# Kernel tuning notes

Hardware: AMD Instinct MI355X
Metric: run time of the kernel (lower is better)

Reference implementation:

```python
import jax, jax.numpy as jnp
import numpy as np

N = 30000      # nodes of type 'A'
IN = 128       # in_channels = hidden*2
H = 64         # hidden_channels
OUT = 64
M = 4          # number of metapaths (seq len for attention)
E = 480000     # edges per relation
NH = 8         # num_heads
HD = OUT // NH # head dim = 8
FF = 2048      # transformer dim_feedforward (torch default)
L = 2          # transformer layers
EPS = 1e-5


def setup_inputs() -> dict:
    key = jax.random.key(0)
    ks = iter(jax.random.split(key, 64))
    nk = lambda: next(ks)
    rn = lambda shape, s=0.05: (jax.random.normal(nk(), shape, jnp.float32) * s)
    x = jax.random.normal(nk(), (N, IN), jnp.float32)
    edge_index = jax.random.randint(nk(), (M, 2, E), 0, N, dtype=jnp.int32)
    counts = jnp.array([3.0, 1.0, 2.0, 2.0], jnp.float32)
    mp_weights = counts / counts.sum()
    inp = dict(x=x, edge_index=edge_index, mp_weights=mp_weights,
               W0=rn((M, H, IN)), b0=rn((M, H)), Wl=rn((M, H, IN)), bl=rn((M, H)),
               W1=rn((M, H, IN)), b1=rn((M, H)), Wo=rn((M, OUT, H)), bo=rn((M, OUT)),
               tinw=rn((L, 3 * OUT, OUT)), tinb=rn((L, 3 * OUT)),
               tow=rn((L, OUT, OUT)), tob=rn((L, OUT)),
               ln1g=jnp.ones((L, OUT)), ln1b=jnp.zeros((L, OUT)),
               ff1w=rn((L, FF, OUT)), ff1b=rn((L, FF)),
               ff2w=rn((L, OUT, FF)), ff2b=rn((L, OUT)),
               ln2g=jnp.ones((L, OUT)), ln2b=jnp.zeros((L, OUT)),
               r1w=rn((OUT, OUT)), r1b=rn((OUT,)), r2w=rn((1, OUT)), r2b=rn((1,)))
    return inp


def _layer_norm(v, g, b):
    mu = v.mean(-1, keepdims=True)
    var = ((v - mu) ** 2).mean(-1, keepdims=True)
    return (v - mu) / jnp.sqrt(var + EPS) * g + b


def reference(x, edge_index, mp_weights, W0, b0, Wl, bl, W1, b1, Wo, bo,
              tinw, tinb, tow, tob, ln1g, ln1b, ff1w, ff1b, ff2w, ff2b,
              ln2g, ln2b, r1w, r1b, r2w, r2b):
    n = x.shape[0]
    # ---- per-metapath GNN: gather + scatter-add + 3 fused linears ----
    embs = []
    for m in range(M):
        src, dst = edge_index[m, 0], edge_index[m, 1]
        # flow='target_to_source', aggr='add': agg[i] = sum_{e: src[e]==i} h[dst[e]]
        agg = jnp.zeros_like(x).at[src].add(x[dst])
        # w_l(agg) + w_0(h) + w_1(x), with h == x (forward passes x=h=h_dict[dst])
        h = jax.nn.relu(agg @ Wl[m].T + bl[m] + x @ (W0[m] + W1[m]).T + (b0[m] + b1[m]))
        embs.append(h @ Wo[m].T + bo[m])  # out_proj on updated start-type feats
    e = jnp.stack(embs, axis=1) * mp_weights[None, :, None]  # (N, M, OUT)

    # ---- 2-layer post-norm TransformerEncoder (batch_first, eval/no dropout) ----
    for l in range(L):
        qkv = e @ tinw[l].T + tinb[l]                       # (N, M, 3*OUT)
        q, k, v = jnp.split(qkv, 3, axis=-1)
        split = lambda t: t.reshape(n, M, NH, HD).transpose(0, 2, 1, 3)  # (N,NH,M,HD)
        q, k, v = split(q), split(k), split(v)
        attn = jax.nn.softmax(jnp.einsum('nhqd,nhkd->nhqk', q, k) / np.float32(np.sqrt(HD)), axis=-1)
        o = jnp.einsum('nhqk,nhkd->nhqd', attn, v).transpose(0, 2, 1, 3).reshape(n, M, OUT)
        o = o @ tow[l].T + tob[l]
        e = _layer_norm(e + o, ln1g[l], ln1b[l])
        f = jax.nn.relu(e @ ff1w[l].T + ff1b[l]) @ ff2w[l].T + ff2b[l]
        e = _layer_norm(e + f, ln2g[l], ln2b[l])

    pooled = e.mean(axis=1)                                  # (N, OUT)
    out = jax.nn.relu(pooled @ r1w.T + r1b) @ r2w.T + r2b    # (N, 1)
    return out[:, 0]
```

## Files before the change

### kernel.cpp

```cpp
#include <hip/hip_runtime.h>
#include <hip/hip_bf16.h>
#include <math.h>

#define N_NODES 30000
#define M_P     4
#define E_EDGES 480000
#define N_TOK   (N_NODES * 4)
#define N_ROWS  (M_P * N_NODES)
#define SLOTS   62
#define LN_EPS  1e-5f

typedef short bf16x8 __attribute__((ext_vector_type(8)));
typedef float f32x4  __attribute__((ext_vector_type(4)));
#define MFMA_B16(a, b, c) __builtin_amdgcn_mfma_f32_16x16x32_bf16(a, b, c, 0, 0, 0)

__device__ inline unsigned short f2bf(float f) {
    union { float f; unsigned u; } v; v.f = f;
    unsigned r = v.u + 0x7fffu + ((v.u >> 16) & 1u);
    return (unsigned short)(r >> 16);
}
__device__ inline unsigned pack2bf(float a, float b) {
    union { __hip_bfloat162 h; unsigned u; } cv;
    cv.h = __float22bfloat162_rn(make_float2(a, b));
    return cv.u;
}
__device__ inline float bf2f(short s) {
    union { unsigned u; float f; } v; v.u = ((unsigned)(unsigned short)s) << 16;
    return v.f;
}

__global__ __launch_bounds__(256, 2) void k_lin_yz(
    const float* __restrict__ x,
    const float* __restrict__ W0, const float* __restrict__ b0,
    const float* __restrict__ Wl, const float* __restrict__ bl,
    const float* __restrict__ W1, const float* __restrict__ b1,
    float* __restrict__ y, float* __restrict__ z)
{
    __shared__ float xT[128][68];
    __shared__ float wT[128][68];
    const int t     = threadIdx.x;
    const int m     = blockIdx.y >> 1;
    const int which = blockIdx.y & 1;
    const int node0 = blockIdx.x * 64;

    #pragma unroll
    for (int i = 0; i < 8; ++i) {
        const int node = (t & 31) + 32 * (i & 1);
        const int kq   = (t >> 5) + 8 * (i >> 1);
        float4 v = make_float4(0.f, 0.f, 0.f, 0.f);
        const int n = node0 + node;
        if (n < N_NODES) v = *(const float4*)(x + n * 128 + kq * 4);
        xT[kq * 4 + 0][node] = v.x; xT[kq * 4 + 1][node] = v.y;
        xT[kq * 4 + 2][node] = v.z; xT[kq * 4 + 3][node] = v.w;
    }
    #pragma unroll
    for (int i = 0; i < 8; ++i) {
        const int h  = (t & 31) + 32 * (i & 1);
        const int kq = (t >> 5) + 8 * (i >> 1);
        float4 v;
        if (which) {
            v = *(const float4*)(W0 + (m * 64 + h) * 128 + kq * 4);
            const float4 v2 = *(const float4*)(W1 + (m * 64 + h) * 128 + kq * 4);
            v.x += v2.x; v.y += v2.y; v.z += v2.z; v.w += v2.w;
        } else {
            v = *(const float4*)(Wl + (m * 64 + h) * 128 + kq * 4);
        }
        wT[kq * 4 + 0][h] = v.x; wT[kq * 4 + 1][h] = v.y;
        wT[kq * 4 + 2][h] = v.z; wT[kq * 4 + 3][h] = v.w;
    }
    __syncthreads();

    const int tx = t & 15, ty = t >> 4;
    const int hb = tx * 4, nb = ty * 4;
    float acc[4][4] = {};
    #pragma unroll 8
    for (int k = 0; k < 128; ++k) {
        const float4 a = *(const float4*)&xT[k][nb];
        const float4 b = *(const float4*)&wT[k][hb];
        acc[0][0] += a.x * b.x; acc[0][1] += a.x * b.y; acc[0][2] += a.x * b.z; acc[0][3] += a.x * b.w;
        acc[1][0] += a.y * b.x; acc[1][1] += a.y * b.y; acc[1][2] += a.y * b.z; acc[1][3] += a.y * b.w;
        acc[2][0] += a.z * b.x; acc[2][1] += a.z * b.y; acc[2][2] += a.z * b.z; acc[2][3] += a.z * b.w;
        acc[3][0] += a.w * b.x; acc[3][1] += a.w * b.y; acc[3][2] += a.w * b.z; acc[3][3] += a.w * b.w;
    }
    float bias[4] = {0.f, 0.f, 0.f, 0.f};
    if (which) {
        #pragma unroll
        for (int j = 0; j < 4; ++j)
            bias[j] = b0[m * 64 + hb + j] + b1[m * 64 + hb + j] + bl[m * 64 + hb + j];
    }
    float* outp = which ? z : y;
    #pragma unroll
    for (int i = 0; i < 4; ++i) {
        const int n = node0 + nb + i;
        if (n < N_NODES) {
            float4 v = make_float4(acc[i][0] + bias[0], acc[i][1] + bias[1],
                                   acc[i][2] + bias[2], acc[i][3] + bias[3]);
            *(float4*)(outp + (m * N_NODES + n) * 64 + hb) = v;
        }
    }
}

__global__ __launch_bounds__(256) void k_fill(
    const int* __restrict__ ei, unsigned short* __restrict__ bins,
    const float* __restrict__ y, float* __restrict__ aggh)
{
    const int base = blockIdx.x * 1024 + threadIdx.x;
    int rows[4], dsts[4];
    #pragma unroll
    for (int i = 0; i < 4; ++i) {
        const int g = base + i * 256;
        const int m = g / E_EDGES;
        const int e = g - m * E_EDGES;
        rows[i] = m * N_NODES + ei[(m * 2) * E_EDGES + e];
        dsts[i] = ei[(m * 2 + 1) * E_EDGES + e];
    }
    int pos[4];
    #pragma unroll
    for (int i = 0; i < 4; ++i)
        pos[i] = atomicAdd((int*)bins + rows[i] * 32, 1);
    #pragma unroll
    for (int i = 0; i < 4; ++i) {
        if (pos[i] < SLOTS) {
            bins[rows[i] * 64 + 2 + pos[i]] = (unsigned short)dsts[i];
        } else {
            const int m = rows[i] / N_NODES;
            const float* yr = y + ((size_t)m * N_NODES + dsts[i]) * 64;
            for (int f = 0; f < 64; ++f)
                unsafeAtomicAdd(&aggh[(size_t)rows[i] * 64 + f], yr[f]);
        }
    }
}

__global__ __launch_bounds__(256) void k_gather(
    const unsigned short* __restrict__ bins,
    const float* __restrict__ y, float* __restrict__ aggh)
{
    const int w = threadIdx.x >> 6, lane = threadIdx.x & 63;
    const int row = blockIdx.x * 4 + w;
    const int m = row / N_NODES;
    const float* ym = y + (size_t)m * N_NODES * 64;
    const int v = bins[row * 64 + lane];
    const int v0 = __shfl(v, 0), v1 = __shfl(v, 1);
    const int tot = (v0 & 0xffff) | (v1 << 16);
    const int cnt = min(tot, SLOTS);
    float acc = (tot > SLOTS) ? aggh[(size_t)row * 64 + lane] : 0.f;
    for (int j = 0; j < cnt; ++j) {
        const int r = __shfl(v, j + 2);
        acc += ym[r * 64 + lane];
    }
    aggh[(size_t)row * 64 + lane] = acc;
}

__global__ __launch_bounds__(256) void k_emb(
    const float* __restrict__ aggh, const float* __restrict__ z,
    const float* __restrict__ Wo, const float* __restrict__ bo,
    const float* __restrict__ mpw, float* __restrict__ e)
{
    __shared__ float hT[64][20];
    __shared__ float WoT[64][64];
    const int t = threadIdx.x;
    const int node0 = blockIdx.x * 16;

    for (int m = 0; m < 4; ++m) {
        #pragma unroll
        for (int i = 0; i < 4; ++i) {
            const int o  = (t & 15) + 16 * i;
            const int kq = t >> 4;
            const float4 v = *(const float4*)(Wo + (m * 64 + o) * 64 + kq * 4);
            WoT[kq * 4 + 0][o] = v.x; WoT[kq * 4 + 1][o] = v.y;
            WoT[kq * 4 + 2][o] = v.z; WoT[kq * 4 + 3][o] = v.w;
        }
        {
            const int node = t & 15, kq = t >> 4;
            const int n = node0 + node;
            const float4 a = *(const float4*)(aggh + (m * N_NODES + n) * 64 + kq * 4);
            const float4 b = *(const float4*)(z + (m * N_NODES + n) * 64 + kq * 4);
            hT[kq * 4 + 0][node] = fmaxf(a.x + b.x, 0.f);
            hT[kq * 4 + 1][node] = fmaxf(a.y + b.y, 0.f);
            hT[kq * 4 + 2][node] = fmaxf(a.z + b.z, 0.f);
            hT[kq * 4 + 3][node] = fmaxf(a.w + b.w, 0.f);
        }
        __syncthreads();
        const int o = t & 63, nl4 = (t >> 6) * 4;
        float acc[4] = {};
        #pragma unroll 8
        for (int k = 0; k < 64; ++k) {
            const float bw = WoT[k][o];
            const float4 a = *(const float4*)&hT[k][nl4];
            acc[0] += a.x * bw; acc[1] += a.y * bw; acc[2] += a.z * bw; acc[3] += a.w * bw;
        }
        const float bb = bo[m * 64 + o];
        const float w  = mpw[m];
        #pragma unroll
        for (int i = 0; i < 4; ++i)
            e[((node0 + nl4 + i) * 4 + m) * 64 + o] = (acc[i] + bb) * w;
        __syncthreads();
    }
}

__global__ __launch_bounds__(256, 2) void k_attn_mfma(
    const float* __restrict__ e,
    const unsigned short* __restrict__ wqkv_s, const float* __restrict__ tinb,
    const unsigned short* __restrict__ tow_s, const float* __restrict__ tob,
    const float* __restrict__ ln1g, const float* __restrict__ ln1b,
    float* __restrict__ eout, int l)
{
    __shared__ __align__(16) short Xl[8192];
    __shared__ __align__(16) short QKV[25600];
    const int t = threadIdx.x;
    const int w = t >> 6, lane = t & 63;
    const int m_ = lane & 15, qc = lane >> 4;
    const int tok0 = blockIdx.x * 128;
    short* Xw = &Xl[w * 2048];
    short* Qw = &QKV[w * 6400];

    #pragma unroll
    for (int i = 0; i < 4; ++i) {
        const int rem = lane + 64 * i;
        const int nt = rem >> 7, h = (rem >> 6) & 1, q = (rem >> 4) & 3, n = rem & 15;
        const int tok = tok0 + w * 32 + nt * 16 + n;
        const int k0 = h * 32 + q * 8;
        float4 a = make_float4(0.f, 0.f, 0.f, 0.f), b = a;
        if (tok < N_TOK) {
            a = *(const float4*)(e + tok * 64 + k0);
            b = *(const float4*)(e + tok * 64 + k0 + 4);
        }
        *(uint4*)&Xw[rem * 8] = make_uint4(pack2bf(a.x, a.y), pack2bf(a.z, a.w),
                                           pack2bf(b.x, b.y), pack2bf(b.z, b.w));
    }

    bf16x8 xb[2][2];
    #pragma unroll
    for (int nt = 0; nt < 2; ++nt)
        #pragma unroll
        for (int h = 0; h < 2; ++h)
            xb[nt][h] = *(const bf16x8*)&Xw[(nt * 2 + h) * 512 + lane * 8];

    const unsigned short* Wq = wqkv_s + l * 12288;
    f32x4 acc[12][2];
    #pragma unroll
    for (int ft = 0; ft < 12; ++ft) {
        const bf16x8 wa0 = *(const bf16x8*)(Wq + (ft * 2 + 0) * 512 + lane * 8);
        const bf16x8 wa1 = *(const bf16x8*)(Wq + (ft * 2 + 1) * 512 + lane * 8);
        const float4 bv = *(const float4*)(tinb + l * 192 + ft * 16 + qc * 4);
        f32x4 c0; c0[0] = bv.x; c0[1] = bv.y; c0[2] = bv.z; c0[3] = bv.w;
        f32x4 c1 = c0;
        c0 = MFMA_B16(wa0, xb[0][0], c0); c0 = MFMA_B16(wa1, xb[0][1], c0);
        c1 = MFMA_B16(wa0, xb[1][0], c1); c1 = MFMA_B16(wa1, xb[1][1], c1);
        acc[ft][0] = c0; acc[ft][1] = c1;
    }
    #pragma unroll
    for (int ft = 0; ft < 12; ++ft)
        #pragma unroll
        for (int nt = 0; nt < 2; ++nt) {
            const int addr = (nt * 16 + m_) * 200 + ft * 16 + qc * 4;
            *(uint2*)&Qw[addr] = make_uint2(pack2bf(acc[ft][nt][0], acc[ft][nt][1]),
                                            pack2bf(acc[ft][nt][2], acc[ft][nt][3]));
        }

    {
        const int node = lane >> 3, head = lane & 7;
        float kk[4][8], vv[4][8];
        #pragma unroll
        for (int j2 = 0; j2 < 4; ++j2) {
            const bf16x8 kr = *(const bf16x8*)&Qw[(node * 4 + j2) * 200 + 64 + head * 8];
            const bf16x8 vr = *(const bf16x8*)&Qw[(node * 4 + j2) * 200 + 128 + head * 8];
            #pragma unroll
            for (int d = 0; d < 8; ++d) { kk[j2][d] = bf2f(kr[d]); vv[j2][d] = bf2f(vr[d]); }
        }
        const float scale = 0.35355339059327373f;
        const int nt = node >> 2, hq = head >> 2, qq = head & 3;
        #pragma unroll
        for (int i = 0; i < 4; ++i) {
            const bf16x8 qr = *(const bf16x8*)&Qw[(node * 4 + i) * 200 + head * 8];
            float q[8];
            #pragma unroll
            for (int d = 0; d < 8; ++d) q[d] = bf2f(qr[d]);
            float s[4];
            #pragma unroll
            for (int j2 = 0; j2 < 4; ++j2) {
                float a2 = 0.f;
                #pragma unroll
                for (int d = 0; d < 8; ++d) a2 += q[d] * kk[j2][d];
                s[j2] = a2 * scale;
            }
            const float mx = fmaxf(fmaxf(s[0], s[1]), fmaxf(s[2], s[3]));
            float p[4], sum = 0.f;
            #pragma unroll
            for (int j2 = 0; j2 < 4; ++j2) { p[j2] = __expf(s[j2] - mx); sum += p[j2]; }
            const float inv = 1.f / sum;
            float o[8];
            #pragma unroll
            for (int d = 0; d < 8; ++d)
                o[d] = (p[0] * vv[0][d] + p[1] * vv[1][d] + p[2] * vv[2][d] + p[3] * vv[3][d]) * inv;
            const int n = (node & 3) * 4 + i;
            *(uint4*)&Xw[(nt * 2 + hq) * 512 + qq * 128 + n * 8] =
                make_uint4(pack2bf(o[0], o[1]), pack2bf(o[2], o[3]),
                           pack2bf(o[4], o[5]), pack2bf(o[6], o[7]));
        }
    }

    bf16x8 ob[2][2];
    #pragma unroll
    for (int nt = 0; nt < 2; ++nt)
        #pragma unroll
        for (int h = 0; h < 2; ++h)
            ob[nt][h] = *(const bf16x8*)&Xw[(nt * 2 + h) * 512 + lane * 8];
    const unsigned short* Tw = tow_s + l * 4096;
    f32x4 acc2[4][2] = {};
    #pragma unroll
    for (int ot = 0; ot < 4; ++ot) {
        const bf16x8 t0 = *(const bf16x8*)(Tw + (ot * 2 + 0) * 512 + lane * 8);
        const bf16x8 t1 = *(const bf16x8*)(Tw + (ot * 2 + 1) * 512 + lane * 8);
        acc2[ot][0] = MFMA_B16(t0, ob[0][0], acc2[ot][0]);
        acc2[ot][0] = MFMA_B16(t1, ob[0][1], acc2[ot][0]);
        acc2[ot][1] = MFMA_B16(t0, ob[1][0], acc2[ot][1]);
        acc2[ot][1] = MFMA_B16(t1, ob[1][1], acc2[ot][1]);
    }

    float4 tbv[4], gv[4], bv2[4];
    #pragma unroll
    for (int ot = 0; ot < 4; ++ot) {
        const int o = l * 64 + ot * 16 + qc * 4;
        tbv[ot] = *(const float4*)(tob + o);
        gv[ot]  = *(const float4*)(ln1g + o);
        bv2[ot] = *(const float4*)(ln1b + o);
    }
    #pragma unroll
    for (int nt = 0; nt < 2; ++nt) {
        const int tok = tok0 + w * 32 + nt * 16 + m_;
        const bool valid = tok < N_TOK;
        float v[4][4];
        float s = 0.f;
        #pragma unroll
        for (int ot = 0; ot < 4; ++ot) {
            float4 rs = make_float4(0.f, 0.f, 0.f, 0.f);
            if (valid) rs = *(const float4*)(e + tok * 64 + ot * 16 + qc * 4);
            v[ot][0] = acc2[ot][nt][0] + tbv[ot].x + rs.x;
            v[ot][1] = acc2[ot][nt][1] + tbv[ot].y + rs.y;
            v[ot][2] = acc2[ot][nt][2] + tbv[ot].z + rs.z;
            v[ot][3] = acc2[ot][nt][3] + tbv[ot].w + rs.w;
            s += v[ot][0] + v[ot][1] + v[ot][2] + v[ot][3];
        }
        s += __shfl_xor(s, 16); s += __shfl_xor(s, 32);
        const float mean = s * (1.f / 64.f);
        float vs = 0.f;
        #pragma unroll
        for (int ot = 0; ot < 4; ++ot)
            #pragma unroll
            for (int r = 0; r < 4; ++r) { v[ot][r] -= mean; vs += v[ot][r] * v[ot][r]; }
        vs += __shfl_xor(vs, 16); vs += __shfl_xor(vs, 32);
        const float rr = rsqrtf(vs * (1.f / 64.f) + LN_EPS);
        if (valid) {
            #pragma unroll
            for (int ot = 0; ot < 4; ++ot) {
                float4 o4 = make_float4(v[ot][0] * rr * gv[ot].x + bv2[ot].x,
                                        v[ot][1] * rr * gv[ot].y + bv2[ot].y,
                                        v[ot][2] * rr * gv[ot].z + bv2[ot].z,
                                        v[ot][3] * rr * gv[ot].w + bv2[ot].w);
                *(float4*)(eout + tok * 64 + ot * 16 + qc * 4) = o4;
            }
        }
    }
}

__global__ __launch_bounds__(256) void k_wshuf(
    const float* __restrict__ ff1w, const float* __restrict__ ff2w,
    const float* __restrict__ tinw, const float* __restrict__ tow,
    unsigned short* __restrict__ w1s, unsigned short* __restrict__ w2s,
    unsigned short* __restrict__ wqkv_s, unsigned short* __restrict__ tow_s)
{
    const int g = blockIdx.x * 256 + threadIdx.x;
    {
        const int l = g >> 17, r2 = g & 131071;
        const int f = r2 >> 6, k = r2 & 63;
        const int c = f >> 6, fc = f & 63, ft = fc >> 4, m = fc & 15;
        const int h = k >> 5, q = (k >> 3) & 3, j = k & 7;
        w1s[l * 131072 + c * 4096 + (ft * 2 + h) * 512 + (q * 16 + m) * 8 + j] = f2bf(ff1w[g]);
    }
    {
        const int l = g >> 17, r2 = g & 131071;
        const int o = r2 >> 11, f = r2 & 2047;
        const int c = f >> 6, fc = f & 63, h = fc >> 5, q = (fc >> 3) & 3, j = fc & 7;
        const int ot = o >> 4, m = o & 15;
        w2s[l * 131072 + c * 4096 + (ot * 2 + h) * 512 + (q * 16 + m) * 8 + j] = f2bf(ff2w[g]);
    }
    if (g < 2 * 192 * 64) {
        const int l = g / 12288, r2 = g - l * 12288;
        const int f = r2 >> 6, k = r2 & 63;
        const int ft = f >> 4, m = f & 15;
        const int h = k >> 5, q = (k >> 3) & 3, j = k & 7;
        wqkv_s[l * 12288 + (ft * 2 + h) * 512 + (q * 16 + m) * 8 + j] = f2bf(tinw[g]);
    }
    if (g < 2 * 64 * 64) {
        const int l = g >> 12, r2 = g & 4095;
        const int o = r2 >> 6, k = r2 & 63;
        const int ot = o >> 4, m = o & 15;
        const int h = k >> 5, q = (k >> 3) & 3, j = k & 7;
        tow_s[l * 4096 + (ot * 2 + h) * 512 + (q * 16 + m) * 8 + j] = f2bf(tow[g]);
    }
}

__global__ __launch_bounds__(256, 3) void k_ffn_mfma(
    const float* __restrict__ e,
    const unsigned short* __restrict__ w1s, const unsigned short* __restrict__ w2s,
    const float* __restrict__ ff1b, const float* __restrict__ ff2b,
    const float* __restrict__ ln2g, const float* __restrict__ ln2b,
    float* __restrict__ eout, int l)
{
    __shared__ __align__(16) short Xl[8192];
    __shared__ __align__(16) short Act[8192];
    __shared__ __align__(16) short Wb[8192];
    const int t = threadIdx.x;
    const int w = t >> 6, lane = t & 63;
    const int m_ = lane & 15, qc = lane >> 4;
    const int tok0 = blockIdx.x * 128;

    #pragma unroll
    for (int i = 0; i < 4; ++i) {
        const int g = t + 256 * i;
        const int gw = g >> 8, rem = g & 255;
        const int nt = rem >> 7, h = (rem >> 6) & 1, q = (rem >> 4) & 3, n = rem & 15;
        const int tok = tok0 + gw * 32 + nt * 16 + n;
        const int k = h * 32 + q * 8;
        float4 a = make_float4(0.f, 0.f, 0.f, 0.f), b = a;
        if (tok < N_TOK) {
            a = *(const float4*)(e + tok * 64 + k);
            b = *(const float4*)(e + tok * 64 + k + 4);
        }
        *(uint4*)&Xl[g * 8] = make_uint4(pack2bf(a.x, a.y), pack2bf(a.z, a.w),
                                         pack2bf(b.x, b.y), pack2bf(b.z, b.w));
    }

    const uint4* gw1 = (const uint4*)(w1s + l * 131072);
    const uint4* gw2 = (const uint4*)(w2s + l * 131072);
    uint4 p0 = gw1[t], p1 = gw1[t + 256], p2 = gw2[t], p3 = gw2[t + 256];
    *(uint4*)&Wb[t * 8] = p0;            *(uint4*)&Wb[(t + 256) * 8] = p1;
    *(uint4*)&Wb[4096 + t * 8] = p2;     *(uint4*)&Wb[4096 + (t + 256) * 8] = p3;

    f32x4 acc[4][2] = {};

    for (int c = 0; c < 32; ++c) {
        __syncthreads();
        if (c < 31) {
            p0 = gw1[(c + 1) * 512 + t];       p1 = gw1[(c + 1) * 512 + t + 256];
            p2 = gw2[(c + 1) * 512 + t];       p3 = gw2[(c + 1) * 512 + t + 256];
        }
        bf16x8 xb[2][2];
        #pragma unroll
        for (int nt = 0; nt < 2; ++nt)
            #pragma unroll
            for (int h = 0; h < 2; ++h)
                xb[nt][h] = *(const bf16x8*)&Xl[w * 2048 + (nt * 2 + h) * 512 + lane * 8];

        #pragma unroll
        for (int ft = 0; ft < 4; ++ft) {
            const bf16x8 wa0 = *(const bf16x8*)&Wb[(ft * 2 + 0) * 512 + lane * 8];
            const bf16x8 wa1 = *(const bf16x8*)&Wb[(ft * 2 + 1) * 512 + lane * 8];
            const float4 bv = *(const float4*)(ff1b + l * 2048 + c * 64 + ft * 16 + qc * 4);
            f32x4 c0; c0[0] = bv.x; c0[1] = bv.y; c0[2] = bv.z; c0[3] = bv.w;
            f32x4 c1 = c0;
            c0 = MFMA_B16(wa0, xb[0][0], c0); c0 = MFMA_B16(wa1, xb[0][1], c0);
            c1 = MFMA_B16(wa0, xb[1][0], c1); c1 = MFMA_B16(wa1, xb[1][1], c1);
            const int ha = ft >> 1, qa = (ft & 1) * 2 + (qc >> 1), jo = (qc & 1) * 4;
            const int boff = w * 2048 + ha * 512 + qa * 128 + m_ * 8 + jo;
            *(uint2*)&Act[boff] =
                make_uint2(pack2bf(fmaxf(c0[0], 0.f), fmaxf(c0[1], 0.f)),
                           pack2bf(fmaxf(c0[2], 0.f), fmaxf(c0[3], 0.f)));
            *(uint2*)&Act[boff + 1024] =
                make_uint2(pack2bf(fmaxf(c1[0], 0.f), fmaxf(c1[1], 0.f)),
                           pack2bf(fmaxf(c1[2], 0.f), fmaxf(c1[3], 0.f)));
        }
        bf16x8 ab[2][2];
        #pragma unroll
        for (int nt = 0; nt < 2; ++nt)
            #pragma unroll
            for (int h = 0; h < 2; ++h)
                ab[nt][h] = *(const bf16x8*)&Act[w * 2048 + (nt * 2 + h) * 512 + lane * 8];
        #pragma unroll
        for (int ot = 0; ot < 4; ++ot) {
            const bf16x8 w20 = *(const bf16x8*)&Wb[4096 + (ot * 2 + 0) * 512 + lane * 8];
            const bf16x8 w21 = *(const bf16x8*)&Wb[4096 + (ot * 2 + 1) * 512 + lane * 8];
            acc[ot][0] = MFMA_B16(w20, ab[0][0], acc[ot][0]);
            acc[ot][0] = MFMA_B16(w21, ab[0][1], acc[ot][0]);
            acc[ot][1] = MFMA_B16(w20, ab[1][0], acc[ot][1]);
            acc[ot][1] = MFMA_B16(w21, ab[1][1], acc[ot][1]);
        }
        __syncthreads();
        if (c < 31) {
            *(uint4*)&Wb[t * 8] = p0;            *(uint4*)&Wb[(t + 256) * 8] = p1;
            *(uint4*)&Wb[4096 + t * 8] = p2;     *(uint4*)&Wb[4096 + (t + 256) * 8] = p3;
        }
    }

    float4 fb2v[4], gv[4], bv2[4];
    #pragma unroll
    for (int ot = 0; ot < 4; ++ot) {
        const int o = l * 64 + ot * 16 + qc * 4;
        fb2v[ot] = *(const float4*)(ff2b + o);
        gv[ot]   = *(const float4*)(ln2g + o);
        bv2[ot]  = *(const float4*)(ln2b + o);
    }
    #pragma unroll
    for (int nt = 0; nt < 2; ++nt) {
        const int tok = tok0 + w * 32 + nt * 16 + m_;
        const bool valid = tok < N_TOK;
        float v[4][4];
        float s = 0.f;
        #pragma unroll
        for (int ot = 0; ot < 4; ++ot) {
            float4 rs = make_float4(0.f, 0.f, 0.f, 0.f);
            if (valid) rs = *(const float4*)(e + tok * 64 + ot * 16 + qc * 4);
            v[ot][0] = acc[ot][nt][0] + fb2v[ot].x + rs.x;
            v[ot][1] = acc[ot][nt][1] + fb2v[ot].y + rs.y;
            v[ot][2] = acc[ot][nt][2] + fb2v[ot].z + rs.z;
            v[ot][3] = acc[ot][nt][3] + fb2v[ot].w + rs.w;
            s += v[ot][0] + v[ot][1] + v[ot][2] + v[ot][3];
        }
        s += __shfl_xor(s, 16); s += __shfl_xor(s, 32);
        const float mean = s * (1.f / 64.f);
        float vs = 0.f;
        #pragma unroll
        for (int ot = 0; ot < 4; ++ot)
            #pragma unroll
            for (int r = 0; r < 4; ++r) { v[ot][r] -= mean; vs += v[ot][r] * v[ot][r]; }
        vs += __shfl_xor(vs, 16); vs += __shfl_xor(vs, 32);
        const float rr = rsqrtf(vs * (1.f / 64.f) + LN_EPS);
        if (valid) {
            #pragma unroll
            for (int ot = 0; ot < 4; ++ot) {
                float4 o4 = make_float4(v[ot][0] * rr * gv[ot].x + bv2[ot].x,
                                        v[ot][1] * rr * gv[ot].y + bv2[ot].y,
                                        v[ot][2] * rr * gv[ot].z + bv2[ot].z,
                                        v[ot][3] * rr * gv[ot].w + bv2[ot].w);
                *(float4*)(eout + tok * 64 + ot * 16 + qc * 4) = o4;
            }
        }
    }
}

__global__ __launch_bounds__(256) void k_reg(
    const float* __restrict__ e,
    const float* __restrict__ r1w, const float* __restrict__ r1b,
    const float* __restrict__ r2w, const float* __restrict__ r2b,
    float* __restrict__ out)
{
    __shared__ float r1T[64][64];
    __shared__ float pld[4][64];
    const int t = threadIdx.x;
    #pragma unroll
    for (int i = 0; i < 4; ++i) {
        const int j  = (t & 15) + 16 * i;
        const int kq = t >> 4;
        const float4 v = *(const float4*)(r1w + j * 64 + kq * 4);
        r1T[kq * 4 + 0][j] = v.x; r1T[kq * 4 + 1][j] = v.y;
        r1T[kq * 4 + 2][j] = v.z; r1T[kq * 4 + 3][j] = v.w;
    }
    const int w = t >> 6, lane = t & 63;
    const int n = blockIdx.x * 4 + w;
    const float p = 0.25f * (e[(n * 4 + 0) * 64 + lane] + e[(n * 4 + 1) * 64 + lane] +
                             e[(n * 4 + 2) * 64 + lane] + e[(n * 4 + 3) * 64 + lane]);
    pld[w][lane] = p;
    __syncthreads();
    float acc = r1b[lane];
    #pragma unroll 8
    for (int k = 0; k < 64; ++k) acc += pld[w][k] * r1T[k][lane];
    acc = fmaxf(acc, 0.f);
    float partial = acc * r2w[lane];
    partial += __shfl_xor(partial, 1);  partial += __shfl_xor(partial, 2);
    partial += __shfl_xor(partial, 4);  partial += __shfl_xor(partial, 8);
    partial += __shfl_xor(partial, 16); partial += __shfl_xor(partial, 32);
    if (lane == 0) out[n] = partial + r2b[0];
}

extern "C" void kernel_launch(void* const* d_in, const int* in_sizes, int n_in,
                              void* d_out, int out_size, void* d_ws, size_t ws_size,
                              hipStream_t stream) {
    const float* x    = (const float*)d_in[0];
    const int*   ei   = (const int*)d_in[1];
    const float* mpw  = (const float*)d_in[2];
    const float* W0   = (const float*)d_in[3];
    const float* b0   = (const float*)d_in[4];
    const float* Wl   = (const float*)d_in[5];
    const float* bl   = (const float*)d_in[6];
    const float* W1   = (const float*)d_in[7];
    const float* b1   = (const float*)d_in[8];
    const float* Wo   = (const float*)d_in[9];
    const float* bo   = (const float*)d_in[10];
    const float* tinw = (const float*)d_in[11];
    const float* tinb = (const float*)d_in[12];
    const float* tow  = (const float*)d_in[13];
    const float* tob  = (const float*)d_in[14];
    const float* ln1g = (const float*)d_in[15];
    const float* ln1b = (const float*)d_in[16];
    const float* ff1w = (const float*)d_in[17];
    const float* ff1b = (const float*)d_in[18];
    const float* ff2w = (const float*)d_in[19];
    const float* ff2b = (const float*)d_in[20];
    const float* ln2g = (const float*)d_in[21];
    const float* ln2b = (const float*)d_in[22];
    const float* r1w  = (const float*)d_in[23];
    const float* r1b  = (const float*)d_in[24];
    const float* r2w  = (const float*)d_in[25];
    const float* r2b  = (const float*)d_in[26];

    const size_t CH = (size_t)M_P * N_NODES * 64;
    float* y    = (float*)d_ws;
    float* zz   = y + CH;
    float* aggh = zz + CH;
    float* e    = aggh + CH;
    unsigned short* w1s    = (unsigned short*)y;
    unsigned short* w2s    = w1s + 262144;
    unsigned short* wqkv_s = w2s + 262144;
    unsigned short* tow_s  = wqkv_s + 24576;
    unsigned short* bins = (unsigned short*)e;

    hipMemsetAsync(bins, 0, (size_t)N_ROWS * 128, stream);
    hipMemsetAsync(aggh, 0, CH * sizeof(float), stream);
    k_lin_yz<<<dim3(469, 8), 256, 0, stream>>>(x, W0, b0, Wl, bl, W1, b1, y, zz);
    k_fill<<<(M_P * E_EDGES) / 1024, 256, 0, stream>>>(ei, bins, y, aggh);
    k_gather<<<N_ROWS / 4, 256, 0, stream>>>(bins, y, aggh);
    k_emb<<<N_NODES / 16, 256, 0, stream>>>(aggh, zz, Wo, bo, mpw, e);
    k_wshuf<<<1024, 256, 0, stream>>>(ff1w, ff2w, tinw, tow, w1s, w2s, wqkv_s, tow_s);
    for (int l = 0; l < 2; ++l) {
        k_attn_mfma<<<(N_TOK + 127) / 128, 256, 0, stream>>>(e, wqkv_s, tinb, tow_s, tob,
                                                             ln1g, ln1b, e, l);
        k_ffn_mfma<<<(N_TOK + 127) / 128, 256, 0, stream>>>(e, w1s, w2s, ff1b, ff2b,
                                                            ln2g, ln2b, e, l);
    }
    k_reg<<<N_NODES / 4, 256, 0, stream>>>(e, r1w, r1b, r2w, r2b, (float*)d_out);
}
```

Measured before the change: 707.8 us.

## Restructure FFN kernel to stream weights from global per wave and shrink edge bins

The FFN kernel now handles 256 tokens per block with 64 tokens per wave. Each wave reads its weight fragments straight from global/L2 instead of staging them through shared memory behind block-wide barriers, and the input X fragments are held in registers for the whole loop. This drops both __syncthreads per chunk and doubles per-wave reuse of each weight fragment, at the cost of more registers (occupancy hint lowered to 2) and more global traffic for weights. Separately, the edge bins shrink from 62 to 30 slots per row, halving the memset and bin footprint. Rows with more than 30 edges spill more often into the slow per-feature atomic fallback.

```diff
diff --git a/kernel.cpp b/kernel.cpp
--- a/kernel.cpp
+++ b/kernel.cpp
@@ -7,7 +7,7 @@
 #define E_EDGES 480000
 #define N_TOK   (N_NODES * 4)
 #define N_ROWS  (M_P * N_NODES)
-#define SLOTS   62
+#define SLOTS   30
 #define LN_EPS  1e-5f
 
 typedef short bf16x8 __attribute__((ext_vector_type(8)));
@@ -117,11 +117,11 @@
     int pos[4];
     #pragma unroll
     for (int i = 0; i < 4; ++i)
-        pos[i] = atomicAdd((int*)bins + rows[i] * 32, 1);
+        pos[i] = atomicAdd((int*)bins + rows[i] * 16, 1);
     #pragma unroll
     for (int i = 0; i < 4; ++i) {
         if (pos[i] < SLOTS) {
-            bins[rows[i] * 64 + 2 + pos[i]] = (unsigned short)dsts[i];
+            bins[rows[i] * 32 + 2 + pos[i]] = (unsigned short)dsts[i];
         } else {
             const int m = rows[i] / N_NODES;
             const float* yr = y + ((size_t)m * N_NODES + dsts[i]) * 64;
@@ -139,7 +139,7 @@
     const int row = blockIdx.x * 4 + w;
     const int m = row / N_NODES;
     const float* ym = y + (size_t)m * N_NODES * 64;
-    const int v = bins[row * 64 + lane];
+    const int v = (lane < 32) ? bins[row * 32 + lane] : 0;
     const int v0 = __shfl(v, 0), v1 = __shfl(v, 1);
     const int tot = (v0 & 0xffff) | (v1 << 16);
     const int cnt = min(tot, SLOTS);
@@ -401,95 +401,87 @@
     }
 }
 
-__global__ __launch_bounds__(256, 3) void k_ffn_mfma(
+__global__ __launch_bounds__(256, 2) void k_ffn_mfma(
     const float* __restrict__ e,
     const unsigned short* __restrict__ w1s, const unsigned short* __restrict__ w2s,
     const float* __restrict__ ff1b, const float* __restrict__ ff2b,
     const float* __restrict__ ln2g, const float* __restrict__ ln2b,
     float* __restrict__ eout, int l)
 {
-    __shared__ __align__(16) short Xl[8192];
-    __shared__ __align__(16) short Act[8192];
-    __shared__ __align__(16) short Wb[8192];
+    __shared__ __align__(16) short Xl[16384];
+    __shared__ __align__(16) short Act[16384];
     const int t = threadIdx.x;
     const int w = t >> 6, lane = t & 63;
     const int m_ = lane & 15, qc = lane >> 4;
-    const int tok0 = blockIdx.x * 128;
-
-    #pragma unroll
-    for (int i = 0; i < 4; ++i) {
-        const int g = t + 256 * i;
-        const int gw = g >> 8, rem = g & 255;
+    const int tok0 = blockIdx.x * 256;
+    short* Xw = &Xl[w * 4096];
+    short* Aw = &Act[w * 4096];
+
+    #pragma unroll
+    for (int i = 0; i < 8; ++i) {
+        const int rem = lane + 64 * i;
         const int nt = rem >> 7, h = (rem >> 6) & 1, q = (rem >> 4) & 3, n = rem & 15;
-        const int tok = tok0 + gw * 32 + nt * 16 + n;
-        const int k = h * 32 + q * 8;
+        const int tok = tok0 + w * 64 + nt * 16 + n;
+        const int k0 = h * 32 + q * 8;
         float4 a = make_float4(0.f, 0.f, 0.f, 0.f), b = a;
         if (tok < N_TOK) {
-            a = *(const float4*)(e + tok * 64 + k);
-            b = *(const float4*)(e + tok * 64 + k + 4);
-        }
-        *(uint4*)&Xl[g * 8] = make_uint4(pack2bf(a.x, a.y), pack2bf(a.z, a.w),
-                                         pack2bf(b.x, b.y), pack2bf(b.z, b.w));
-    }
-
-    const uint4* gw1 = (const uint4*)(w1s + l * 131072);
-    const uint4* gw2 = (const uint4*)(w2s + l * 131072);
-    uint4 p0 = gw1[t], p1 = gw1[t + 256], p2 = gw2[t], p3 = gw2[t + 256];
-    *(uint4*)&Wb[t * 8] = p0;            *(uint4*)&Wb[(t + 256) * 8] = p1;
-    *(uint4*)&Wb[4096 + t * 8] = p2;     *(uint4*)&Wb[4096 + (t + 256) * 8] = p3;
-
-    f32x4 acc[4][2] = {};
-
+            a = *(const float4*)(e + tok * 64 + k0);
+            b = *(const float4*)(e + tok * 64 + k0 + 4);
+        }
+        *(uint4*)&Xw[rem * 8] = make_uint4(pack2bf(a.x, a.y), pack2bf(a.z, a.w),
+                                           pack2bf(b.x, b.y), pack2bf(b.z, b.w));
+    }
+
+    bf16x8 xb[4][2];
+    #pragma unroll
+    for (int nt = 0; nt < 4; ++nt)
+        #pragma unroll
+        for (int h = 0; h < 2; ++h)
+            xb[nt][h] = *(const bf16x8*)&Xw[(nt * 2 + h) * 512 + lane * 8];
+
+    const unsigned short* gw1 = w1s + l * 131072;
+    const unsigned short* gw2 = w2s + l * 131072;
+    f32x4 acc[4][4] = {};
+
+    #pragma unroll 2
     for (int c = 0; c < 32; ++c) {
-        __syncthreads();
-        if (c < 31) {
-            p0 = gw1[(c + 1) * 512 + t];       p1 = gw1[(c + 1) * 512 + t + 256];
-            p2 = gw2[(c + 1) * 512 + t];       p3 = gw2[(c + 1) * 512 + t + 256];
-        }
-        bf16x8 xb[2][2];
-        #pragma unroll
-        for (int nt = 0; nt < 2; ++nt)
+        const unsigned short* W1c = gw1 + c * 4096;
+        const unsigned short* W2c = gw2 + c * 4096;
+        #pragma unroll
+        for (int ft = 0; ft < 4; ++ft) {
+            const bf16x8 wa0 = *(const bf16x8*)(W1c + (ft * 2 + 0) * 512 + lane * 8);
+            const bf16x8 wa1 = *(const bf16x8*)(W1c + (ft * 2 + 1) * 512 + lane * 8);
+            const float4 bv = *(const float4*)(ff1b + l * 2048 + c * 64 + ft * 16 + qc * 4);
+            f32x4 cc[4];
+            #pragma unroll
+            for (int nt = 0; nt < 4; ++nt) {
+                f32x4 c0; c0[0] = bv.x; c0[1] = bv.y; c0[2] = bv.z; c0[3] = bv.w;
+                c0 = MFMA_B16(wa0, xb[nt][0], c0);
+                c0 = MFMA_B16(wa1, xb[nt][1], c0);
+                cc[nt] = c0;
+            }
+            const int ha = ft >> 1, qa = (ft & 1) * 2 + (qc >> 1), jo = (qc & 1) * 4;
+            #pragma unroll
+            for (int nt = 0; nt < 4; ++nt)
+                *(uint2*)&Aw[(nt * 2 + ha) * 512 + qa * 128 + m_ * 8 + jo] =
+                    make_uint2(pack2bf(fmaxf(cc[nt][0], 0.f), fmaxf(cc[nt][1], 0.f)),
+                               pack2bf(fmaxf(cc[nt][2], 0.f), fmaxf(cc[nt][3], 0.f)));
+        }
+        bf16x8 ab[4][2];
+        #pragma unroll
+        for (int nt = 0; nt < 4; ++nt)
             #pragma unroll
             for (int h = 0; h < 2; ++h)
-                xb[nt][h] = *(const bf16x8*)&Xl[w * 2048 + (nt * 2 + h) * 512 + lane * 8];
-
-        #pragma unroll
-        for (int ft = 0; ft < 4; ++ft) {
-            const bf16x8 wa0 = *(const bf16x8*)&Wb[(ft * 2 + 0) * 512 + lane * 8];
-            const bf16x8 wa1 = *(const bf16x8*)&Wb[(ft * 2 + 1) * 512 + lane * 8];
-            const float4 bv = *(const float4*)(ff1b + l * 2048 + c * 64 + ft * 16 + qc * 4);
-            f32x4 c0; c0[0] = bv.x; c0[1] = bv.y; c0[2] = bv.z; c0[3] = bv.w;
-            f32x4 c1 = c0;
-            c0 = MFMA_B16(wa0, xb[0][0], c0); c0 = MFMA_B16(wa1, xb[0][1], c0);
-            c1 = MFMA_B16(wa0, xb[1][0], c1); c1 = MFMA_B16(wa1, xb[1][1], c1);
-            const int ha = ft >> 1, qa = (ft & 1) * 2 + (qc >> 1), jo = (qc & 1) * 4;
-            const int boff = w * 2048 + ha * 512 + qa * 128 + m_ * 8 + jo;
-            *(uint2*)&Act[boff] =
-                make_uint2(pack2bf(fmaxf(c0[0], 0.f), fmaxf(c0[1], 0.f)),
-                           pack2bf(fmaxf(c0[2], 0.f), fmaxf(c0[3], 0.f)));
-            *(uint2*)&Act[boff + 1024] =
-                make_uint2(pack2bf(fmaxf(c1[0], 0.f), fmaxf(c1[1], 0.f)),
-                           pack2bf(fmaxf(c1[2], 0.f), fmaxf(c1[3], 0.f)));
-        }
-        bf16x8 ab[2][2];
-        #pragma unroll
-        for (int nt = 0; nt < 2; ++nt)
-            #pragma unroll
-            for (int h = 0; h < 2; ++h)
-                ab[nt][h] = *(const bf16x8*)&Act[w * 2048 + (nt * 2 + h) * 512 + lane * 8];
+                ab[nt][h] = *(const bf16x8*)&Aw[(nt * 2 + h) * 512 + lane * 8];
         #pragma unroll
         for (int ot = 0; ot < 4; ++ot) {
-            const bf16x8 w20 = *(const bf16x8*)&Wb[4096 + (ot * 2 + 0) * 512 + lane * 8];
-            const bf16x8 w21 = *(const bf16x8*)&Wb[4096 + (ot * 2 + 1) * 512 + lane * 8];
-            acc[ot][0] = MFMA_B16(w20, ab[0][0], acc[ot][0]);
-            acc[ot][0] = MFMA_B16(w21, ab[0][1], acc[ot][0]);
-            acc[ot][1] = MFMA_B16(w20, ab[1][0], acc[ot][1]);
-            acc[ot][1] = MFMA_B16(w21, ab[1][1], acc[ot][1]);
-        }
-        __syncthreads();
-        if (c < 31) {
-            *(uint4*)&Wb[t * 8] = p0;            *(uint4*)&Wb[(t + 256) * 8] = p1;
-            *(uint4*)&Wb[4096 + t * 8] = p2;     *(uint4*)&Wb[4096 + (t + 256) * 8] = p3;
+            const bf16x8 w20 = *(const bf16x8*)(W2c + (ot * 2 + 0) * 512 + lane * 8);
+            const bf16x8 w21 = *(const bf16x8*)(W2c + (ot * 2 + 1) * 512 + lane * 8);
+            #pragma unroll
+            for (int nt = 0; nt < 4; ++nt) {
+                acc[ot][nt] = MFMA_B16(w20, ab[nt][0], acc[ot][nt]);
+                acc[ot][nt] = MFMA_B16(w21, ab[nt][1], acc[ot][nt]);
+            }
         }
     }
 
@@ -502,8 +494,8 @@
         bv2[ot]  = *(const float4*)(ln2b + o);
     }
     #pragma unroll
-    for (int nt = 0; nt < 2; ++nt) {
-        const int tok = tok0 + w * 32 + nt * 16 + m_;
+    for (int nt = 0; nt < 4; ++nt) {
+        const int tok = tok0 + w * 64 + nt * 16 + m_;
         const bool valid = tok < N_TOK;
         float v[4][4];
         float s = 0.f;
@@ -615,7 +607,7 @@
     unsigned short* tow_s  = wqkv_s + 24576;
     unsigned short* bins = (unsigned short*)e;
 
-    hipMemsetAsync(bins, 0, (size_t)N_ROWS * 128, stream);
+    hipMemsetAsync(bins, 0, (size_t)N_ROWS * 64, stream);
     hipMemsetAsync(aggh, 0, CH * sizeof(float), stream);
     k_lin_yz<<<dim3(469, 8), 256, 0, stream>>>(x, W0, b0, Wl, bl, W1, b1, y, zz);
     k_fill<<<(M_P * E_EDGES) / 1024, 256, 0, stream>>>(ei, bins, y, aggh);
@@ -625,7 +617,7 @@
     for (int l = 0; l < 2; ++l) {
         k_attn_mfma<<<(N_TOK + 127) / 128, 256, 0, stream>>>(e, wqkv_s, tinb, tow_s, tob,
                                                              ln1g, ln1b, e, l);
-        k_ffn_mfma<<<(N_TOK + 127) / 128, 256, 0, stream>>>(e, w1s, w2s, ff1b, ff2b,
+        k_ffn_mfma<<<(N_TOK + 255) / 256, 256, 0, stream>>>(e, w1s, w2s, ff1b, ff2b,
                                                             ln2g, ln2b, e, l);
     }
     k_reg<<<N_NODES / 4, 256, 0, stream>>>(e, r1w, r1b, r2w, r2b, (float*)d_out);
```

New measurement: 748.2 us. +5.7%, slower.

## Load MFMA input fragments directly from global, shrink LDS and edge bins

Applied to the files above, without the earlier changes.

The attention and FFN kernels now build their bf16 input fragments straight from global memory into registers instead of staging through an LDS tile. The QKV scratch is split into separate Q/K and V buffers with tighter strides. Together these cut shared-memory use, and the launch-bound occupancy hints are raised accordingly. Edge bins shrink from 62 to 30 slots per row, which halves the bins memset and gather footprint. The trade-off is that more high-degree rows overflow into the slow per-feature atomic fallback path.

```diff
diff --git a/kernel.cpp b/kernel.cpp
--- a/kernel.cpp
+++ b/kernel.cpp
@@ -7,7 +7,7 @@
 #define E_EDGES 480000
 #define N_TOK   (N_NODES * 4)
 #define N_ROWS  (M_P * N_NODES)
-#define SLOTS   62
+#define SLOTS   30
 #define LN_EPS  1e-5f
 
 typedef short bf16x8 __attribute__((ext_vector_type(8)));
@@ -27,6 +27,12 @@
 __device__ inline float bf2f(short s) {
     union { unsigned u; float f; } v; v.u = ((unsigned)(unsigned short)s) << 16;
     return v.f;
+}
+__device__ inline bf16x8 mk_frag(const float4& a, const float4& b) {
+    union { uint4 u; bf16x8 v; } cv;
+    cv.u = make_uint4(pack2bf(a.x, a.y), pack2bf(a.z, a.w),
+                      pack2bf(b.x, b.y), pack2bf(b.z, b.w));
+    return cv.v;
 }
 
 __global__ __launch_bounds__(256, 2) void k_lin_yz(
@@ -117,11 +123,11 @@
     int pos[4];
     #pragma unroll
     for (int i = 0; i < 4; ++i)
-        pos[i] = atomicAdd((int*)bins + rows[i] * 32, 1);
+        pos[i] = atomicAdd((int*)bins + rows[i] * 16, 1);
     #pragma unroll
     for (int i = 0; i < 4; ++i) {
         if (pos[i] < SLOTS) {
-            bins[rows[i] * 64 + 2 + pos[i]] = (unsigned short)dsts[i];
+            bins[rows[i] * 32 + 2 + pos[i]] = (unsigned short)dsts[i];
         } else {
             const int m = rows[i] / N_NODES;
             const float* yr = y + ((size_t)m * N_NODES + dsts[i]) * 64;
@@ -139,7 +145,7 @@
     const int row = blockIdx.x * 4 + w;
     const int m = row / N_NODES;
     const float* ym = y + (size_t)m * N_NODES * 64;
-    const int v = bins[row * 64 + lane];
+    const int v = (lane < 32) ? bins[row * 32 + lane] : 0;
     const int v0 = __shfl(v, 0), v1 = __shfl(v, 1);
     const int tot = (v0 & 0xffff) | (v1 << 16);
     const int cnt = min(tot, SLOTS);
@@ -198,43 +204,36 @@
     }
 }
 
-__global__ __launch_bounds__(256, 2) void k_attn_mfma(
+__global__ __launch_bounds__(256, 3) void k_attn_mfma(
     const float* __restrict__ e,
     const unsigned short* __restrict__ wqkv_s, const float* __restrict__ tinb,
     const unsigned short* __restrict__ tow_s, const float* __restrict__ tob,
     const float* __restrict__ ln1g, const float* __restrict__ ln1b,
     float* __restrict__ eout, int l)
 {
-    __shared__ __align__(16) short Xl[8192];
-    __shared__ __align__(16) short QKV[25600];
+    __shared__ __align__(16) short QK[17408];
+    __shared__ __align__(16) short Vb[9216];
     const int t = threadIdx.x;
     const int w = t >> 6, lane = t & 63;
     const int m_ = lane & 15, qc = lane >> 4;
     const int tok0 = blockIdx.x * 128;
-    short* Xw = &Xl[w * 2048];
-    short* Qw = &QKV[w * 6400];
-
-    #pragma unroll
-    for (int i = 0; i < 4; ++i) {
-        const int rem = lane + 64 * i;
-        const int nt = rem >> 7, h = (rem >> 6) & 1, q = (rem >> 4) & 3, n = rem & 15;
-        const int tok = tok0 + w * 32 + nt * 16 + n;
-        const int k0 = h * 32 + q * 8;
-        float4 a = make_float4(0.f, 0.f, 0.f, 0.f), b = a;
-        if (tok < N_TOK) {
-            a = *(const float4*)(e + tok * 64 + k0);
-            b = *(const float4*)(e + tok * 64 + k0 + 4);
-        }
-        *(uint4*)&Xw[rem * 8] = make_uint4(pack2bf(a.x, a.y), pack2bf(a.z, a.w),
-                                           pack2bf(b.x, b.y), pack2bf(b.z, b.w));
-    }
+    short* QKw = &QK[w * 4352];
+    short* Vw  = &Vb[w * 2304];
 
     bf16x8 xb[2][2];
     #pragma unroll
     for (int nt = 0; nt < 2; ++nt)
         #pragma unroll
-        for (int h = 0; h < 2; ++h)
-            xb[nt][h] = *(const bf16x8*)&Xw[(nt * 2 + h) * 512 + lane * 8];
+        for (int h = 0; h < 2; ++h) {
+            const int tok = tok0 + w * 32 + nt * 16 + m_;
+            const int k0 = h * 32 + qc * 8;
+            float4 a = make_float4(0.f, 0.f, 0.f, 0.f), b = a;
+            if (tok < N_TOK) {
+                a = *(const float4*)(e + tok * 64 + k0);
+                b = *(const float4*)(e + tok * 64 + k0 + 4);
+            }
+            xb[nt][h] = mk_frag(a, b);
+        }
 
     const unsigned short* Wq = wqkv_s + l * 12288;
     f32x4 acc[12][2];
@@ -250,38 +249,45 @@
         acc[ft][0] = c0; acc[ft][1] = c1;
     }
     #pragma unroll
-    for (int ft = 0; ft < 12; ++ft)
+    for (int ft = 0; ft < 8; ++ft)
         #pragma unroll
         for (int nt = 0; nt < 2; ++nt) {
-            const int addr = (nt * 16 + m_) * 200 + ft * 16 + qc * 4;
-            *(uint2*)&Qw[addr] = make_uint2(pack2bf(acc[ft][nt][0], acc[ft][nt][1]),
+            const int addr = (nt * 16 + m_) * 136 + ft * 16 + qc * 4;
+            *(uint2*)&QKw[addr] = make_uint2(pack2bf(acc[ft][nt][0], acc[ft][nt][1]),
+                                             pack2bf(acc[ft][nt][2], acc[ft][nt][3]));
+        }
+    #pragma unroll
+    for (int ft = 8; ft < 12; ++ft)
+        #pragma unroll
+        for (int nt = 0; nt < 2; ++nt) {
+            const int addr = (nt * 16 + m_) * 72 + (ft - 8) * 16 + qc * 4;
+            *(uint2*)&Vw[addr] = make_uint2(pack2bf(acc[ft][nt][0], acc[ft][nt][1]),
                                             pack2bf(acc[ft][nt][2], acc[ft][nt][3]));
         }
 
     {
         const int node = lane >> 3, head = lane & 7;
-        float kk[4][8], vv[4][8];
+        float kk[4][8], vv[4][8], qv[4][8];
         #pragma unroll
         for (int j2 = 0; j2 < 4; ++j2) {
-            const bf16x8 kr = *(const bf16x8*)&Qw[(node * 4 + j2) * 200 + 64 + head * 8];
-            const bf16x8 vr = *(const bf16x8*)&Qw[(node * 4 + j2) * 200 + 128 + head * 8];
-            #pragma unroll
-            for (int d = 0; d < 8; ++d) { kk[j2][d] = bf2f(kr[d]); vv[j2][d] = bf2f(vr[d]); }
+            const bf16x8 kr = *(const bf16x8*)&QKw[(node * 4 + j2) * 136 + 64 + head * 8];
+            const bf16x8 vr = *(const bf16x8*)&Vw[(node * 4 + j2) * 72 + head * 8];
+            const bf16x8 qr = *(const bf16x8*)&QKw[(node * 4 + j2) * 136 + head * 8];
+            #pragma unroll
+            for (int d = 0; d < 8; ++d) {
+                kk[j2][d] = bf2f(kr[d]); vv[j2][d] = bf2f(vr[d]); qv[j2][d] = bf2f(qr[d]);
+            }
         }
         const float scale = 0.35355339059327373f;
-        const int nt = node >> 2, hq = head >> 2, qq = head & 3;
+        const int nt2 = node >> 2, hq = head >> 2, qq = head & 3;
         #pragma unroll
         for (int i = 0; i < 4; ++i) {
-            const bf16x8 qr = *(const bf16x8*)&Qw[(node * 4 + i) * 200 + head * 8];
-            float q[8];
-            #pragma unroll
-            for (int d = 0; d < 8; ++d) q[d] = bf2f(qr[d]);
             float s[4];
             #pragma unroll
             for (int j2 = 0; j2 < 4; ++j2) {
                 float a2 = 0.f;
                 #pragma unroll
-                for (int d = 0; d < 8; ++d) a2 += q[d] * kk[j2][d];
+                for (int d = 0; d < 8; ++d) a2 += qv[i][d] * kk[j2][d];
                 s[j2] = a2 * scale;
             }
             const float mx = fmaxf(fmaxf(s[0], s[1]), fmaxf(s[2], s[3]));
@@ -294,7 +300,7 @@
             for (int d = 0; d < 8; ++d)
                 o[d] = (p[0] * vv[0][d] + p[1] * vv[1][d] + p[2] * vv[2][d] + p[3] * vv[3][d]) * inv;
             const int n = (node & 3) * 4 + i;
-            *(uint4*)&Xw[(nt * 2 + hq) * 512 + qq * 128 + n * 8] =
+            *(uint4*)&QKw[(nt2 * 2 + hq) * 512 + qq * 128 + n * 8] =
                 make_uint4(pack2bf(o[0], o[1]), pack2bf(o[2], o[3]),
                            pack2bf(o[4], o[5]), pack2bf(o[6], o[7]));
         }
@@ -305,7 +311,7 @@
     for (int nt = 0; nt < 2; ++nt)
         #pragma unroll
         for (int h = 0; h < 2; ++h)
-            ob[nt][h] = *(const bf16x8*)&Xw[(nt * 2 + h) * 512 + lane * 8];
+            ob[nt][h] = *(const bf16x8*)&QKw[(nt * 2 + h) * 512 + lane * 8];
     const unsigned short* Tw = tow_s + l * 4096;
     f32x4 acc2[4][2] = {};
     #pragma unroll
@@ -401,36 +407,35 @@
     }
 }
 
-__global__ __launch_bounds__(256, 3) void k_ffn_mfma(
+__global__ __launch_bounds__(256, 4) void k_ffn_mfma(
     const float* __restrict__ e,
     const unsigned short* __restrict__ w1s, const unsigned short* __restrict__ w2s,
     const float* __restrict__ ff1b, const float* __restrict__ ff2b,
     const float* __restrict__ ln2g, const float* __restrict__ ln2b,
     float* __restrict__ eout, int l)
 {
-    __shared__ __align__(16) short Xl[8192];
     __shared__ __align__(16) short Act[8192];
     __shared__ __align__(16) short Wb[8192];
     const int t = threadIdx.x;
     const int w = t >> 6, lane = t & 63;
     const int m_ = lane & 15, qc = lane >> 4;
     const int tok0 = blockIdx.x * 128;
-
-    #pragma unroll
-    for (int i = 0; i < 4; ++i) {
-        const int g = t + 256 * i;
-        const int gw = g >> 8, rem = g & 255;
-        const int nt = rem >> 7, h = (rem >> 6) & 1, q = (rem >> 4) & 3, n = rem & 15;
-        const int tok = tok0 + gw * 32 + nt * 16 + n;
-        const int k = h * 32 + q * 8;
-        float4 a = make_float4(0.f, 0.f, 0.f, 0.f), b = a;
-        if (tok < N_TOK) {
-            a = *(const float4*)(e + tok * 64 + k);
-            b = *(const float4*)(e + tok * 64 + k + 4);
-        }
-        *(uint4*)&Xl[g * 8] = make_uint4(pack2bf(a.x, a.y), pack2bf(a.z, a.w),
-                                         pack2bf(b.x, b.y), pack2bf(b.z, b.w));
-    }
+    short* Aw = &Act[w * 2048];
+
+    bf16x8 xb[2][2];
+    #pragma unroll
+    for (int nt = 0; nt < 2; ++nt)
+        #pragma unroll
+        for (int h = 0; h < 2; ++h) {
+            const int tok = tok0 + w * 32 + nt * 16 + m_;
+            const int k0 = h * 32 + qc * 8;
+            float4 a = make_float4(0.f, 0.f, 0.f, 0.f), b = a;
+            if (tok < N_TOK) {
+                a = *(const float4*)(e + tok * 64 + k0);
+                b = *(const float4*)(e + tok * 64 + k0 + 4);
+            }
+            xb[nt][h] = mk_frag(a, b);
+        }
 
     const uint4* gw1 = (const uint4*)(w1s + l * 131072);
     const uint4* gw2 = (const uint4*)(w2s + l * 131072);
@@ -446,13 +451,6 @@
             p0 = gw1[(c + 1) * 512 + t];       p1 = gw1[(c + 1) * 512 + t + 256];
             p2 = gw2[(c + 1) * 512 + t];       p3 = gw2[(c + 1) * 512 + t + 256];
         }
-        bf16x8 xb[2][2];
-        #pragma unroll
-        for (int nt = 0; nt < 2; ++nt)
-            #pragma unroll
-            for (int h = 0; h < 2; ++h)
-                xb[nt][h] = *(const bf16x8*)&Xl[w * 2048 + (nt * 2 + h) * 512 + lane * 8];
-
         #pragma unroll
         for (int ft = 0; ft < 4; ++ft) {
             const bf16x8 wa0 = *(const bf16x8*)&Wb[(ft * 2 + 0) * 512 + lane * 8];
@@ -463,11 +461,11 @@
             c0 = MFMA_B16(wa0, xb[0][0], c0); c0 = MFMA_B16(wa1, xb[0][1], c0);
             c1 = MFMA_B16(wa0, xb[1][0], c1); c1 = MFMA_B16(wa1, xb[1][1], c1);
             const int ha = ft >> 1, qa = (ft & 1) * 2 + (qc >> 1), jo = (qc & 1) * 4;
-            const int boff = w * 2048 + ha * 512 + qa * 128 + m_ * 8 + jo;
-            *(uint2*)&Act[boff] =
+            const int boff = ha * 512 + qa * 128 + m_ * 8 + jo;
+            *(uint2*)&Aw[boff] =
                 make_uint2(pack2bf(fmaxf(c0[0], 0.f), fmaxf(c0[1], 0.f)),
                            pack2bf(fmaxf(c0[2], 0.f), fmaxf(c0[3], 0.f)));
-            *(uint2*)&Act[boff + 1024] =
+            *(uint2*)&Aw[boff + 1024] =
                 make_uint2(pack2bf(fmaxf(c1[0], 0.f), fmaxf(c1[1], 0.f)),
                            pack2bf(fmaxf(c1[2], 0.f), fmaxf(c1[3], 0.f)));
         }
@@ -476,7 +474,7 @@
         for (int nt = 0; nt < 2; ++nt)
             #pragma unroll
             for (int h = 0; h < 2; ++h)
-                ab[nt][h] = *(const bf16x8*)&Act[w * 2048 + (nt * 2 + h) * 512 + lane * 8];
+                ab[nt][h] = *(const bf16x8*)&Aw[(nt * 2 + h) * 512 + lane * 8];
         #pragma unroll
         for (int ot = 0; ot < 4; ++ot) {
             const bf16x8 w20 = *(const bf16x8*)&Wb[4096 + (ot * 2 + 0) * 512 + lane * 8];
@@ -615,7 +613,7 @@
     unsigned short* tow_s  = wqkv_s + 24576;
     unsigned short* bins = (unsigned short*)e;
 
-    hipMemsetAsync(bins, 0, (size_t)N_ROWS * 128, stream);
+    hipMemsetAsync(bins, 0, (size_t)N_ROWS * 64, stream);
     hipMemsetAsync(aggh, 0, CH * sizeof(float), stream);
     k_lin_yz<<<dim3(469, 8), 256, 0, stream>>>(x, W0, b0, Wl, bl, W1, b1, y, zz);
     k_fill<<<(M_P * E_EDGES) / 1024, 256, 0, stream>>>(ei, bins, y, aggh);
```

Measured after the change: 693.5 us. -2.0%, faster.
